# Kernel tuning notes

Measured on AMD Instinct MI355X. Metric: run time of the kernel, lower is better.

The kernel has to match this reference:

```python
import jax, jax.numpy as jnp
import numpy as np

N_ITEMS = 50001   # n_items + 1 (padding row 0)
DIM = 256         # item_embedding_dim == hidden_size
PURPOSES = 3
TAU = 0.1
SEQ_LEN = 50
BATCH = 128
EPS = 0.01
STDV = 1.0 / np.sqrt(DIM)


def setup_inputs() -> dict:
    key = jax.random.key(0)
    ks = jax.random.split(key, 7)
    u = lambda k, s: jax.random.uniform(k, s, jnp.float32, -STDV, STDV)
    emb = u(ks[0], (N_ITEMS, DIM)).at[0].set(0.0)  # padding_idx=0
    emb_purpose = u(ks[1], (PURPOSES, DIM))
    w_ih = u(ks[2], (PURPOSES, 3 * DIM, DIM))
    w_hh = u(ks[3], (PURPOSES, 3 * DIM, DIM))
    b_ih = u(ks[4], (PURPOSES, 3 * DIM))
    b_hh = u(ks[5], (PURPOSES, 3 * DIM))
    seq = jax.random.randint(ks[6], (SEQ_LEN, BATCH), 0, N_ITEMS)
    return {"seq": seq, "emb": emb, "emb_purpose": emb_purpose,
            "w_ih": w_ih, "w_hh": w_hh, "b_ih": b_ih, "b_hh": b_hh}


def _psru(w_ih, w_hh, b_ih, b_hh, seq_embs, concen):
    # seq_embs: [B,S,D], concen: [B,S] -> final hidden [B,D]
    B = seq_embs.shape[0]
    H = w_hh.shape[1]

    def cell(h, xs):
        x, c = xs  # x: [B,D], c: [B]
        gi = x @ w_ih.T + b_ih
        gh = h @ w_hh.T + b_hh
        i_r, i_i, i_n = jnp.split(gi, 3, axis=1)
        h_r, h_i, h_n = jnp.split(gh, 3, axis=1)
        resetgate = jax.nn.sigmoid(i_r + h_r)
        inputgate = jax.nn.sigmoid(i_i + h_i)
        newgate = jnp.tanh(i_n + resetgate * h_n)
        cf = jnp.where(c >= EPS, c, 0.0)[:, None]  # concen gating
        hy = h - cf * inputgate * (h - newgate)
        return hy, None

    h0 = jnp.zeros((B, H), seq_embs.dtype)
    hN, _ = jax.lax.scan(cell, h0, (jnp.swapaxes(seq_embs, 0, 1), concen.T))
    return hN


def reference(seq, emb, emb_purpose, w_ih, w_hh, b_ih, b_hh):
    s = seq.T                               # [B,S]
    mask = (s != 0).astype(emb.dtype)       # padding mask
    seq_embs = emb[s]                       # [B,S,D]
    concen_score = jnp.einsum('bsd,pd->bsp', seq_embs, emb_purpose)
    concen_w = jax.nn.softmax(concen_score / TAU, axis=2) * mask[:, :, None]
    # run one PSRU per purpose, batched with vmap over the purpose axis
    hn = jax.vmap(_psru, in_axes=(0, 0, 0, 0, None, 2))(
        w_ih, w_hh, b_ih, b_hh, seq_embs, concen_w)   # [P,B,D]
    # target = arange(n_items) -> pos_embs = full embedding table
    tcw = jax.nn.softmax(emb @ emb_purpose.T, axis=1)  # [T,P]
    # scores[b,t] = sum_p tcw[t,p] * <hn[p,b,:], emb[t,:]>
    scores = jnp.einsum('pbd,td,tp->bt', hn, emb, tcw)  # [B,T]
    return scores
```

## Files before the change

### kernel.cpp

```cpp
#include <hip/hip_runtime.h>
#include <hip/hip_bf16.h>

#define S_LEN 50
#define BATCH 128
#define DIM 256
#define NITEMS 50001
#define NPAD 50048
#define GDIM 768
#define NSEQ 6400

typedef __attribute__((ext_vector_type(8))) short short8;
typedef __attribute__((ext_vector_type(4))) short short4_;
typedef __attribute__((ext_vector_type(4))) float float4_;

static __device__ __forceinline__ unsigned short f2bf(float x){
  union { float f; unsigned u; } v; v.f = x;
  unsigned r = v.u + 0x7FFFu + ((v.u >> 16) & 1u);
  return (unsigned short)(r >> 16);
}
static __device__ __forceinline__ float bf2f(unsigned short h){
  union { unsigned u; float f; } v; v.u = ((unsigned)h) << 16;
  return v.f;
}
static __device__ __forceinline__ float rcpf_(float x){ return __builtin_amdgcn_rcpf(x); }
static __device__ __forceinline__ float exp2f_(float x){ return __builtin_amdgcn_exp2f(x); }

__global__ __launch_bounds__(256) void k_prep(
        const float* __restrict__ wih, unsigned short* __restrict__ wihT,
        const float* __restrict__ whh, unsigned short* __restrict__ whh_bf,
        const float* __restrict__ emb, const float* __restrict__ embp,
        const int* __restrict__ seq, unsigned short* __restrict__ xT,
        float* __restrict__ cfb){
  __shared__ unsigned short sT[8192];
  int bid = blockIdx.x;
  int tid = threadIdx.x;
  if (bid < 576){
    int i = bid*256 + tid;
    float4_ y = ((const float4_*)whh)[i];
    short4_ v;
    #pragma unroll
    for (int j=0;j<4;j++) v[j] = (short)f2bf(y[j]);
    ((short4_*)whh_bf)[i] = v;
    return;
  }
  int w = tid >> 6, lane = tid & 63;
  int r16 = w*4 + (lane >> 4);
  int c0  = lane & 15;
  if (bid < 720){
    int bx = bid - 576;
    const float4_* er = (const float4_*)(wih + (size_t)(bx*16 + r16)*DIM);
    #pragma unroll
    for (int k=0;k<4;k++){
      float4_ v = er[k*16 + c0];
      short4_ o;
      #pragma unroll
      for (int jj=0;jj<4;jj++) o[jj] = (short)f2bf(v[jj]);
      int di = k*64 + c0*4;
      int kf = di >> 5, qd = (di >> 3) & 3, j = di & 7;
      *(short4_*)(sT + (kf*64 + r16 + qd*16)*8 + j) = o;
    }
    __syncthreads();
    unsigned short* dst = wihT + (size_t)bx*4096 + tid*16;
    *(short8*)(dst)     = *(const short8*)(sT + tid*16);
    *(short8*)(dst + 8) = *(const short8*)(sT + tid*16 + 8);
    return;
  }
  {
    int bx = bid - 720;
    int wid = bx*16 + r16;
    int s = wid >> 7, b = wid & 127;
    int item = seq[s*BATCH + b];
    const float4_* er = (const float4_*)(emb + (size_t)item*DIM);
    const float4_* pp = (const float4_*)embp;
    float d0=0.f, d1=0.f, d2=0.f;
    #pragma unroll
    for (int k=0;k<4;k++){
      float4_ v = er[k*16 + c0];
      short4_ o;
      #pragma unroll
      for (int jj=0;jj<4;jj++) o[jj] = (short)f2bf(v[jj]);
      int di = k*64 + c0*4;
      int kf = di >> 5, qd = (di >> 3) & 3, j = di & 7;
      *(short4_*)(sT + (kf*64 + r16 + qd*16)*8 + j) = o;
      float4_ e0 = pp[k*16 + c0], e1 = pp[64 + k*16 + c0], e2 = pp[128 + k*16 + c0];
      #pragma unroll
      for (int jj=0;jj<4;jj++){ d0 += v[jj]*e0[jj]; d1 += v[jj]*e1[jj]; d2 += v[jj]*e2[jj]; }
    }
    #pragma unroll
    for (int off=1; off<16; off<<=1){
      d0 += __shfl_xor(d0,off); d1 += __shfl_xor(d1,off); d2 += __shfl_xor(d2,off);
    }
    if (c0 == 0){
      float m = fmaxf(d0, fmaxf(d1,d2));
      float a0 = __expf((d0-m)*10.f), a1 = __expf((d1-m)*10.f), a2 = __expf((d2-m)*10.f);
      float inv = (item != 0) ? rcpf_(a0+a1+a2) : 0.f;
      float cc0 = a0*inv, cc1 = a1*inv, cc2 = a2*inv;
      cfb[wid]          = (cc0 >= 0.01f) ? cc0 : 0.f;
      cfb[NSEQ + wid]   = (cc1 >= 0.01f) ? cc1 : 0.f;
      cfb[2*NSEQ + wid] = (cc2 >= 0.01f) ? cc2 : 0.f;
    }
    __syncthreads();
    unsigned short* dst = xT + (size_t)bx*4096 + tid*16;
    *(short8*)(dst)     = *(const short8*)(sT + tid*16);
    *(short8*)(dst + 8) = *(const short8*)(sT + tid*16 + 8);
  }
}

__global__ __launch_bounds__(256) void k_gi(const unsigned short* __restrict__ xT,
        const unsigned short* __restrict__ wihT, const float* __restrict__ bih,
        const float* __restrict__ bhh, unsigned short* __restrict__ gi2){
  extern __shared__ unsigned short sB[];
  int bid = blockIdx.x;
  int tid = threadIdx.x;
  int nb  = bid % 6;
  int rem = bid / 6;
  int yy  = rem % 100;
  int p   = rem / 100;
  const unsigned short* Bsrc = wihT + (size_t)(p*48 + nb*8)*4096;
  #pragma unroll
  for (int r = 0; r < 16; r++){
    int c16 = r*256 + tid;
    *(short8*)(sB + c16*8) = *(const short8*)(Bsrc + c16*8);
  }
  __syncthreads();
  int wv = tid >> 6;
  int lane = tid & 63;
  int col = lane & 15, q = lane >> 4;
  int mt = yy*4 + wv;
  float4_ z4 = {0.f,0.f,0.f,0.f};
  float4_ acc[8];
  #pragma unroll
  for (int t=0;t<8;t++) acc[t] = z4;
  #pragma unroll
  for (int kf=0; kf<8; kf++){
    short8 a = *(const short8*)(xT + (((size_t)mt*8 + kf)*64 + lane)*8);
    #pragma unroll
    for (int nt=0; nt<8; nt++){
      short8 bb = *(const short8*)(sB + ((nt*8 + kf)*64 + lane)*8);
      acc[nt] = __builtin_amdgcn_mfma_f32_16x16x32_bf16(a, bb, acc[nt], 0, 0, 0);
    }
  }
  int s     = yy >> 1;
  int slice = (yy & 1)*4 + wv;
  size_t X = (size_t)(p*S_LEN + s)*8 + slice;
  int g = (nb*8) >> 4;
  #pragma unroll
  for (int nt=0; nt<8; nt++){
    int nn = nb*8 + nt;
    int wc = (nn >> 1) & 7;
    int tt = nn & 1;
    int n  = nn*16 + col;
    float bv = bih[p*GDIM + n] + ((g < 2) ? bhh[p*GDIM + n] : 0.f);
    short4_ ov;
    #pragma unroll
    for (int i=0;i<4;i++) ov[i] = (short)f2bf(acc[nt][i] + bv);
    *(short4_*)(gi2 + X*12288 + (size_t)(g*16 + wc*2 + tt)*256 + lane*4) = ov;
  }
}

__global__ __launch_bounds__(512) __attribute__((amdgpu_waves_per_eu(2, 2)))
void k_rnn(const unsigned short* __restrict__ whh_bf,
         const unsigned short* __restrict__ gi2, const float* __restrict__ bhh,
         const float* __restrict__ cfb, unsigned short* __restrict__ hnT,
         const float* __restrict__ emb, const float* __restrict__ embp,
         unsigned short* __restrict__ embT, float* __restrict__ tcw){
  extern __shared__ char lds[];
  int bid = blockIdx.x;
  int tid = threadIdx.x;
  if (bid >= 24){
    int sub = tid >> 8;
    int t2  = tid & 255;
    unsigned short* sT = (unsigned short*)lds + sub*8192;
    int w = t2 >> 6, lane = t2 & 63;
    int r16 = w*4 + (lane >> 4);
    int c0  = lane & 15;
    int bx2 = (bid - 24)*2 + sub;
    int row = bx2*16 + r16;
    bool valid = row < NITEMS;
    const float4_* er = (const float4_*)(emb + (size_t)row*DIM);
    const float4_* pp = (const float4_*)embp;
    float d0=0.f, d1=0.f, d2=0.f;
    #pragma unroll
    for (int k=0;k<4;k++){
      float4_ v = valid ? er[k*16 + c0] : float4_{0.f,0.f,0.f,0.f};
      short4_ o;
      #pragma unroll
      for (int jj=0;jj<4;jj++) o[jj] = (short)f2bf(v[jj]);
      int di = k*64 + c0*4;
      int kf = di >> 5, qd = (di >> 3) & 3, j = di & 7;
      *(short4_*)(sT + (kf*64 + r16 + qd*16)*8 + j) = o;
      float4_ e0 = pp[k*16 + c0], e1 = pp[64 + k*16 + c0], e2 = pp[128 + k*16 + c0];
      #pragma unroll
      for (int jj=0;jj<4;jj++){ d0 += v[jj]*e0[jj]; d1 += v[jj]*e1[jj]; d2 += v[jj]*e2[jj]; }
    }
    #pragma unroll
    for (int off=1; off<16; off<<=1){
      d0 += __shfl_xor(d0,off); d1 += __shfl_xor(d1,off); d2 += __shfl_xor(d2,off);
    }
    if (c0 == 0 && valid){
      float m = fmaxf(d0, fmaxf(d1,d2));
      float a0 = __expf(d0-m), a1 = __expf(d1-m), a2 = __expf(d2-m);
      float inv = rcpf_(a0+a1+a2);
      tcw[row*3+0] = a0*inv; tcw[row*3+1] = a1*inv; tcw[row*3+2] = a2*inv;
    }
    __syncthreads();
    unsigned short* dst = embT + (size_t)bx2*4096 + t2*16;
    *(short8*)(dst)     = *(const short8*)(sT + t2*16);
    *(short8*)(dst + 8) = *(const short8*)(sT + t2*16 + 8);
    return;
  }
  float* cfs = (float*)(lds + 147456);
  int p  = bid >> 3;
  int slice = bid & 7;
  int b0 = slice * 16;
  int w = tid >> 6, lane = tid & 63;
  int col = lane & 15;
  int q = lane >> 4;
  int kq = q * 8;
  const unsigned short* Wp = whh_bf + (size_t)p*GDIM*DIM;

  for (int i = tid; i < 8192; i += 512) ((unsigned short*)lds)[i] = 0;
  for (int i = tid; i < 800; i += 512) cfs[i] = cfb[p*NSEQ + (i>>4)*BATCH + b0 + (i&15)];
  {
    const unsigned short* Wn = Wp + (size_t)512*DIM;
    #pragma unroll
    for (int r = 0; r < 16; r++){
      int j = r*512 + tid;
      int kf = j >> 10, row = (j >> 2) & 255, qs = j & 3;
      short8 v = *(const short8*)(Wn + (size_t)row*DIM + kf*32 + ((qs ^ ((row>>1)&3)) << 3));
      *(short8*)(lds + 16384 + j*16) = v;
    }
  }

  float bias_n0 = bhh[p*GDIM + 512 + w*32 + col];
  float bias_n1 = bhh[p*GDIM + 512 + w*32 + 16 + col];

  short8 Bf[8][4];
  #pragma unroll
  for (int kf=0; kf<8; kf++){
    #pragma unroll
    for (int t=0;t<4;t++){
      int gc = (t>>1)*256 + w*32 + (t&1)*16 + col;
      Bf[kf][t] = *(const short8*)(Wp + ((size_t)gc << 8) + kf*32 + kq);
      asm volatile("" : "+a"(Bf[kf][t]));
    }
  }
  const char* wn0 = lds + 16384 + (size_t)(w*32 + col)*64 + ((q ^ ((col>>1)&3)) << 4);
  const char* wn1 = wn0 + 16*64;
  int swz  = (lane & 7) << 4;
  float hreg[2][4];
  #pragma unroll
  for (int t=0;t<2;t++){
    #pragma unroll
    for (int i=0;i<4;i++) hreg[t][i] = 0.f;
  }
  const size_t GSTRIDE = (size_t)8*12288;
  const unsigned short* gbase =
      gi2 + ((size_t)p*S_LEN*8 + slice)*12288 + (size_t)(w*2)*256 + lane*4;
  short4_ cur[6], nxt[6];
  #pragma unroll
  for (int t=0;t<6;t++)
    cur[t] = *(const short4_*)(gbase + (t>>1)*4096 + (t&1)*256);
  __syncthreads();

  const float K1 = -1.442695041f;
  const float K2 =  2.885390082f;
  float4_ z4 = {0.f,0.f,0.f,0.f};
  for (int s = 0; s < S_LEN; s++){
    int rbuf = s & 1, wbuf = rbuf ^ 1;
    int sn = (s+1 < S_LEN) ? s+1 : 0;
    const unsigned short* gnp = gbase + (size_t)sn*GSTRIDE;
    #pragma unroll
    for (int t=0;t<6;t++)
      nxt[t] = *(const short4_*)(gnp + (t>>1)*4096 + (t&1)*256);
    float4_ acc[6];
    #pragma unroll
    for (int t=0;t<6;t++) acc[t] = z4;
    const char* hrow = lds + rbuf*8192 + col*512;
    #pragma unroll
    for (int kf=0; kf<8; kf++){
      int ko = (kf*64 + q*16);
      short8 a = *(const short8*)(hrow + (ko ^ swz));
      #pragma unroll
      for (int t=0;t<4;t++)
        acc[t] = __builtin_amdgcn_mfma_f32_16x16x32_bf16(a, Bf[kf][t], acc[t], 0, 0, 0);
      short8 b4 = *(const short8*)(wn0 + kf*16384);
      acc[4] = __builtin_amdgcn_mfma_f32_16x16x32_bf16(a, b4, acc[4], 0, 0, 0);
      short8 b5 = *(const short8*)(wn1 + kf*16384);
      acc[5] = __builtin_amdgcn_mfma_f32_16x16x32_bf16(a, b5, acc[5], 0, 0, 0);
    }
    float4_ cfv = *(const float4_*)(cfs + s*16 + 4*q);
    char* wbase = lds + wbuf*8192;
    int d0b = 2*(w*32 + col);
    #pragma unroll
    for (int i=0;i<4;i++){
      int rb = 4*q + i;
      float hy01[2];
      #pragma unroll
      for (int t=0;t<2;t++){
        float bn = t ? bias_n1 : bias_n0;
        float r = rcpf_(1.f + exp2f_(K1*(bf2f((unsigned short)cur[t][i])   + acc[t][i])));
        float z = rcpf_(1.f + exp2f_(K1*(bf2f((unsigned short)cur[2+t][i]) + acc[2+t][i])));
        float pre = bf2f((unsigned short)cur[4+t][i]) + r*(acc[4+t][i] + bn);
        float n = 1.f - 2.f*rcpf_(exp2f_(K2*pre) + 1.f);
        float ho = hreg[t][i];
        float hy = ho - cfv[i]*z*(ho - n);
        hreg[t][i] = hy;
        hy01[t] = hy;
      }
      unsigned pk;
      asm("v_cvt_pk_bf16_f32 %0, %1, %2" : "=v"(pk) : "v"(hy01[0]), "v"(hy01[1]));
      char* rowp = wbase + rb*512;
      int sw = (rb & 7) << 4;
      *(unsigned short*)(rowp + (d0b ^ sw))        = (unsigned short)pk;
      *(unsigned short*)(rowp + ((d0b + 32) ^ sw)) = (unsigned short)(pk >> 16);
    }
    #pragma unroll
    for (int t=0;t<6;t++) cur[t] = nxt[t];
    __syncthreads();
  }
  #pragma unroll
  for (int t=0; t<2; t++){
    int d  = w*32 + t*16 + col;
    int kf = d >> 5;
    int qd = (d >> 3) & 3;
    int j  = d & 7;
    #pragma unroll
    for (int i=0; i<4; i++){
      int rb = 4*q + i;
      hnT[(((size_t)p*8 + slice)*8 + kf)*512 + (size_t)(rb + qd*16)*8 + j] = f2bf(hreg[t][i]);
    }
  }
}

__global__ __launch_bounds__(256) void k_score(const unsigned short* __restrict__ embT,
        const unsigned short* __restrict__ hnT, const float* __restrict__ tcw,
        float* __restrict__ out){
  __shared__ float sm[64*129];
  int w = threadIdx.x >> 6, lane = threadIdx.x & 63;
  int col = lane & 15, q = lane >> 4;
  int t16 = blockIdx.x*4 + w;
  int trow = t16*16 + col;
  float4_ z4 = {0.f,0.f,0.f,0.f};
  float4_ acc[3][8];
  #pragma unroll
  for (int p=0;p<3;p++){
    #pragma unroll
    for (int m=0;m<8;m++) acc[p][m] = z4;
  }
  #pragma unroll
  for (int kf=0; kf<8; kf++){
    short8 bb = *(const short8*)(embT + (((size_t)t16*8 + kf)*64 + lane)*8);
    #pragma unroll
    for (int p=0;p<3;p++){
      #pragma unroll
      for (int m=0;m<8;m++){
        short8 a = *(const short8*)(hnT + ((((size_t)p*8 + m)*8 + kf)*512) + lane*8);
        acc[p][m] = __builtin_amdgcn_mfma_f32_16x16x32_bf16(a, bb, acc[p][m], 0, 0, 0);
      }
    }
  }
  float w0=0.f, w1=0.f, w2=0.f;
  if (trow < NITEMS){ w0 = tcw[trow*3+0]; w1 = tcw[trow*3+1]; w2 = tcw[trow*3+2]; }
  #pragma unroll
  for (int m=0;m<8;m++){
    #pragma unroll
    for (int i=0;i<4;i++){
      sm[(w*16 + col)*129 + m*16 + 4*q + i] =
          w0*acc[0][m][i] + w1*acc[1][m][i] + w2*acc[2][m][i];
    }
  }
  __syncthreads();
  int trowW = blockIdx.x*64 + lane;
  if (trowW < NITEMS){
    float* orow = out + trowW;
    #pragma unroll 4
    for (int c=0; c<32; c++){
      int b = w*32 + c;
      orow[(size_t)b*NITEMS] = sm[lane*129 + b];
    }
  }
}

extern "C" void kernel_launch(void* const* d_in, const int* in_sizes, int n_in,
                              void* d_out, int out_size, void* d_ws, size_t ws_size,
                              hipStream_t stream) {
  const int*   seq  = (const int*)d_in[0];
  const float* emb  = (const float*)d_in[1];
  const float* embp = (const float*)d_in[2];
  const float* wih  = (const float*)d_in[3];
  const float* whh  = (const float*)d_in[4];
  const float* bih  = (const float*)d_in[5];
  const float* bhh  = (const float*)d_in[6];
  float* out = (float*)d_out;

  char* ws = (char*)d_ws;
  size_t off = 0;
  auto alloc = [&](size_t bytes) -> void* {
    void* r = ws + off; off += (bytes + 255) & ~(size_t)255; return r;
  };
  unsigned short* embT   = (unsigned short*)alloc((size_t)NPAD*DIM*2);
  unsigned short* xT     = (unsigned short*)alloc((size_t)NSEQ*DIM*2);
  unsigned short* wihT   = (unsigned short*)alloc((size_t)3*GDIM*DIM*2);
  unsigned short* whh_bf = (unsigned short*)alloc((size_t)3*GDIM*DIM*2);
  unsigned short* gi2    = (unsigned short*)alloc((size_t)3*NSEQ*GDIM*2);
  float* tcw = (float*)alloc((size_t)NITEMS*3*4);
  float* cfb = (float*)alloc((size_t)3*NSEQ*4);
  unsigned short* hnT = (unsigned short*)alloc((size_t)3*BATCH*DIM*2);

  k_prep<<<1120, 256, 0, stream>>>(wih, wihT, whh, whh_bf, emb, embp, seq, xT, cfb);

  (void)hipFuncSetAttribute((const void*)k_gi,
        hipFuncAttributeMaxDynamicSharedMemorySize, 65536);
  k_gi<<<1800, 256, 65536, stream>>>(xT, wihT, bih, bhh, gi2);

  (void)hipFuncSetAttribute((const void*)k_rnn,
        hipFuncAttributeMaxDynamicSharedMemorySize, 150656);
  k_rnn<<<1588, 512, 150656, stream>>>(whh_bf, gi2, bhh, cfb, hnT,
                                       emb, embp, embT, tcw);

  k_score<<<NPAD/64, 256, 0, stream>>>(embT, hnT, tcw, out);
}
```

Measured before the change: 181.6 us.

## Fuse prep kernel into input-gate GEMM, converting fp32 operands on the fly

Removes the separate k_prep launch and its intermediate bf16 buffers (xT, wihT). The gate GEMM now loads fp32 W_ih and gathers the embedding rows directly, converting them to bf16 into LDS and registers. Extra blocks in the same grid handle the W_hh conversion and the concentration-weight softmax. This saves one launch and a round trip through global memory, but each GEMM block now reads fp32 data and repeats the bf16 conversion, and W_ih is reloaded many times across blocks.

```diff
diff --git a/kernel.cpp b/kernel.cpp
--- a/kernel.cpp
+++ b/kernel.cpp
@@ -25,17 +25,44 @@
 static __device__ __forceinline__ float rcpf_(float x){ return __builtin_amdgcn_rcpf(x); }
 static __device__ __forceinline__ float exp2f_(float x){ return __builtin_amdgcn_exp2f(x); }
 
-__global__ __launch_bounds__(256) void k_prep(
-        const float* __restrict__ wih, unsigned short* __restrict__ wihT,
-        const float* __restrict__ whh, unsigned short* __restrict__ whh_bf,
+__global__ __launch_bounds__(256) void k_gi(const int* __restrict__ seq,
         const float* __restrict__ emb, const float* __restrict__ embp,
-        const int* __restrict__ seq, unsigned short* __restrict__ xT,
+        const float* __restrict__ wih, const float* __restrict__ whh,
+        const float* __restrict__ bih, const float* __restrict__ bhh,
+        unsigned short* __restrict__ gi2, unsigned short* __restrict__ whh_bf,
         float* __restrict__ cfb){
-  __shared__ unsigned short sT[8192];
+  extern __shared__ unsigned short sB[];
   int bid = blockIdx.x;
   int tid = threadIdx.x;
-  if (bid < 576){
-    int i = bid*256 + tid;
+  if (bid >= 2376){
+    int bx = bid - 2376;
+    int wv = tid >> 6, lane = tid & 63;
+    const float4_* pp = (const float4_*)embp;
+    float4_ e0 = pp[lane], e1 = pp[64+lane], e2 = pp[128+lane];
+    for (int it = 0; it < 16; ++it){
+      int wid = bx*64 + wv*16 + it;
+      int s = wid >> 7, b = wid & 127;
+      int item = seq[s*BATCH + b];
+      float4_ v = ((const float4_*)(emb + (size_t)item*DIM))[lane];
+      float d0=0.f,d1=0.f,d2=0.f;
+      #pragma unroll
+      for (int j=0;j<4;j++){ d0 += v[j]*e0[j]; d1 += v[j]*e1[j]; d2 += v[j]*e2[j]; }
+      #pragma unroll
+      for (int off=32; off; off>>=1){ d0 += __shfl_xor(d0,off); d1 += __shfl_xor(d1,off); d2 += __shfl_xor(d2,off); }
+      if (lane == 0){
+        float m = fmaxf(d0, fmaxf(d1,d2));
+        float a0 = __expf((d0-m)*10.f), a1 = __expf((d1-m)*10.f), a2 = __expf((d2-m)*10.f);
+        float inv = (item != 0) ? rcpf_(a0+a1+a2) : 0.f;
+        float c0 = a0*inv, c1 = a1*inv, c2 = a2*inv;
+        cfb[wid]          = (c0 >= 0.01f) ? c0 : 0.f;
+        cfb[NSEQ + wid]   = (c1 >= 0.01f) ? c1 : 0.f;
+        cfb[2*NSEQ + wid] = (c2 >= 0.01f) ? c2 : 0.f;
+      }
+    }
+    return;
+  }
+  if (bid >= 1800){
+    int i = (bid - 1800)*256 + tid;
     float4_ y = ((const float4_*)whh)[i];
     short4_ v;
     #pragma unroll
@@ -43,107 +70,54 @@
     ((short4_*)whh_bf)[i] = v;
     return;
   }
-  int w = tid >> 6, lane = tid & 63;
-  int r16 = w*4 + (lane >> 4);
-  int c0  = lane & 15;
-  if (bid < 720){
-    int bx = bid - 576;
-    const float4_* er = (const float4_*)(wih + (size_t)(bx*16 + r16)*DIM);
-    #pragma unroll
-    for (int k=0;k<4;k++){
-      float4_ v = er[k*16 + c0];
-      short4_ o;
-      #pragma unroll
-      for (int jj=0;jj<4;jj++) o[jj] = (short)f2bf(v[jj]);
-      int di = k*64 + c0*4;
-      int kf = di >> 5, qd = (di >> 3) & 3, j = di & 7;
-      *(short4_*)(sT + (kf*64 + r16 + qd*16)*8 + j) = o;
-    }
-    __syncthreads();
-    unsigned short* dst = wihT + (size_t)bx*4096 + tid*16;
-    *(short8*)(dst)     = *(const short8*)(sT + tid*16);
-    *(short8*)(dst + 8) = *(const short8*)(sT + tid*16 + 8);
-    return;
-  }
-  {
-    int bx = bid - 720;
-    int wid = bx*16 + r16;
-    int s = wid >> 7, b = wid & 127;
-    int item = seq[s*BATCH + b];
-    const float4_* er = (const float4_*)(emb + (size_t)item*DIM);
-    const float4_* pp = (const float4_*)embp;
-    float d0=0.f, d1=0.f, d2=0.f;
-    #pragma unroll
-    for (int k=0;k<4;k++){
-      float4_ v = er[k*16 + c0];
-      short4_ o;
-      #pragma unroll
-      for (int jj=0;jj<4;jj++) o[jj] = (short)f2bf(v[jj]);
-      int di = k*64 + c0*4;
-      int kf = di >> 5, qd = (di >> 3) & 3, j = di & 7;
-      *(short4_*)(sT + (kf*64 + r16 + qd*16)*8 + j) = o;
-      float4_ e0 = pp[k*16 + c0], e1 = pp[64 + k*16 + c0], e2 = pp[128 + k*16 + c0];
-      #pragma unroll
-      for (int jj=0;jj<4;jj++){ d0 += v[jj]*e0[jj]; d1 += v[jj]*e1[jj]; d2 += v[jj]*e2[jj]; }
-    }
-    #pragma unroll
-    for (int off=1; off<16; off<<=1){
-      d0 += __shfl_xor(d0,off); d1 += __shfl_xor(d1,off); d2 += __shfl_xor(d2,off);
-    }
-    if (c0 == 0){
-      float m = fmaxf(d0, fmaxf(d1,d2));
-      float a0 = __expf((d0-m)*10.f), a1 = __expf((d1-m)*10.f), a2 = __expf((d2-m)*10.f);
-      float inv = (item != 0) ? rcpf_(a0+a1+a2) : 0.f;
-      float cc0 = a0*inv, cc1 = a1*inv, cc2 = a2*inv;
-      cfb[wid]          = (cc0 >= 0.01f) ? cc0 : 0.f;
-      cfb[NSEQ + wid]   = (cc1 >= 0.01f) ? cc1 : 0.f;
-      cfb[2*NSEQ + wid] = (cc2 >= 0.01f) ? cc2 : 0.f;
-    }
-    __syncthreads();
-    unsigned short* dst = xT + (size_t)bx*4096 + tid*16;
-    *(short8*)(dst)     = *(const short8*)(sT + tid*16);
-    *(short8*)(dst + 8) = *(const short8*)(sT + tid*16 + 8);
-  }
-}
-
-__global__ __launch_bounds__(256) void k_gi(const unsigned short* __restrict__ xT,
-        const unsigned short* __restrict__ wihT, const float* __restrict__ bih,
-        const float* __restrict__ bhh, unsigned short* __restrict__ gi2){
-  extern __shared__ unsigned short sB[];
-  int bid = blockIdx.x;
-  int tid = threadIdx.x;
-  int nb  = bid % 6;
-  int rem = bid / 6;
-  int yy  = rem % 100;
-  int p   = rem / 100;
-  const unsigned short* Bsrc = wihT + (size_t)(p*48 + nb*8)*4096;
-  #pragma unroll
-  for (int r = 0; r < 16; r++){
-    int c16 = r*256 + tid;
-    *(short8*)(sB + c16*8) = *(const short8*)(Bsrc + c16*8);
-  }
-  __syncthreads();
+  int p   = bid / 600;
+  int rem = bid % 600;
+  int yy  = rem / 6;
+  int nb  = rem % 6;
   int wv = tid >> 6;
   int lane = tid & 63;
   int col = lane & 15, q = lane >> 4;
+  for (int r = 0; r < 16; ++r){
+    int c = r*256 + tid;
+    int nt = c >> 9, kf = (c >> 6) & 7, l = c & 63;
+    const float* src = wih + ((size_t)p*GDIM + (size_t)(nb*8 + nt)*16 + (l & 15))*DIM
+                           + kf*32 + (l >> 4)*8;
+    float4_ f0 = *(const float4_*)(src);
+    float4_ f1 = *(const float4_*)(src + 4);
+    short8 o;
+    #pragma unroll
+    for (int j=0;j<4;j++){ o[j] = (short)f2bf(f0[j]); o[4+j] = (short)f2bf(f1[j]); }
+    *(short8*)(sB + (size_t)c*8) = o;
+  }
   int mt = yy*4 + wv;
+  int wid = mt*16 + col;
+  int item = seq[(wid >> 7)*BATCH + (wid & 127)];
+  const float* xr = emb + (size_t)item*DIM + q*8;
+  short8 Af[8];
+  #pragma unroll
+  for (int kf=0; kf<8; kf++){
+    float4_ f0 = *(const float4_*)(xr + kf*32);
+    float4_ f1 = *(const float4_*)(xr + kf*32 + 4);
+    #pragma unroll
+    for (int j=0;j<4;j++){ Af[kf][j] = (short)f2bf(f0[j]); Af[kf][4+j] = (short)f2bf(f1[j]); }
+  }
+  __syncthreads();
   float4_ z4 = {0.f,0.f,0.f,0.f};
   float4_ acc[8];
   #pragma unroll
   for (int t=0;t<8;t++) acc[t] = z4;
   #pragma unroll
   for (int kf=0; kf<8; kf++){
-    short8 a = *(const short8*)(xT + (((size_t)mt*8 + kf)*64 + lane)*8);
     #pragma unroll
     for (int nt=0; nt<8; nt++){
       short8 bb = *(const short8*)(sB + ((nt*8 + kf)*64 + lane)*8);
-      acc[nt] = __builtin_amdgcn_mfma_f32_16x16x32_bf16(a, bb, acc[nt], 0, 0, 0);
+      acc[nt] = __builtin_amdgcn_mfma_f32_16x16x32_bf16(Af[kf], bb, acc[nt], 0, 0, 0);
     }
   }
   int s     = yy >> 1;
   int slice = (yy & 1)*4 + wv;
   size_t X = (size_t)(p*S_LEN + s)*8 + slice;
-  int g = (nb*8) >> 4;
+  int g = nb >> 1;
   #pragma unroll
   for (int nt=0; nt<8; nt++){
     int nn = nb*8 + nt;
@@ -400,19 +374,16 @@
     void* r = ws + off; off += (bytes + 255) & ~(size_t)255; return r;
   };
   unsigned short* embT   = (unsigned short*)alloc((size_t)NPAD*DIM*2);
-  unsigned short* xT     = (unsigned short*)alloc((size_t)NSEQ*DIM*2);
-  unsigned short* wihT   = (unsigned short*)alloc((size_t)3*GDIM*DIM*2);
   unsigned short* whh_bf = (unsigned short*)alloc((size_t)3*GDIM*DIM*2);
   unsigned short* gi2    = (unsigned short*)alloc((size_t)3*NSEQ*GDIM*2);
   float* tcw = (float*)alloc((size_t)NITEMS*3*4);
   float* cfb = (float*)alloc((size_t)3*NSEQ*4);
   unsigned short* hnT = (unsigned short*)alloc((size_t)3*BATCH*DIM*2);
 
-  k_prep<<<1120, 256, 0, stream>>>(wih, wihT, whh, whh_bf, emb, embp, seq, xT, cfb);
-
   (void)hipFuncSetAttribute((const void*)k_gi,
         hipFuncAttributeMaxDynamicSharedMemorySize, 65536);
-  k_gi<<<1800, 256, 65536, stream>>>(xT, wihT, bih, bhh, gi2);
+  k_gi<<<2476, 256, 65536, stream>>>(seq, emb, embp, wih, whh, bih, bhh,
+                                     gi2, whh_bf, cfb);
 
   (void)hipFuncSetAttribute((const void*)k_rnn,
         hipFuncAttributeMaxDynamicSharedMemorySize, 150656);
```

After: 215.1 us. +18.5%, slower.
